# Kernel optimization log

Measured on AMD Instinct MI355X. Metric: run time of the kernel, lower is better.

The kernel has to match this reference:

```python
import jax, jax.numpy as jnp
import numpy as np

IN_F = 4096
OUT_F = 4096
BATCH = 4096


def _dequantize(q, mn, mx):
    # Faithful to dequantize_to_float32: per-tensor affine using the *observed*
    # integer min/max of the stored tensor.
    q_min = q.min()
    q_max = q.max()
    scale = (mx - mn) / (q_max - q_min).astype(jnp.float32)
    return (q - q_min).astype(jnp.float32) * scale + mn


def setup_inputs() -> dict:
    key = jax.random.key(0)
    k1, k2, k3 = jax.random.split(key, 3)
    x = jax.random.normal(k1, (BATCH, IN_F), dtype=jnp.float32)
    # int8-valued weights/bias stored as int32 (same math; dequant uses tensor min/max)
    weight_q = jax.random.randint(k2, (OUT_F, IN_F), -128, 128, dtype=jnp.int32)
    bias_q = jax.random.randint(k3, (OUT_F,), -128, 128, dtype=jnp.int32)
    # per-tensor float range recorded at quantization time (original scales by 255 first,
    # so these ranges are on the scaled tensor; any floats work for correctness testing)
    weight_min = jnp.float32(-4.2)
    weight_max = jnp.float32(4.5)
    bias_min = jnp.float32(-1.3)
    bias_max = jnp.float32(1.1)
    return {
        "x": x,
        "weight_q": weight_q,
        "bias_q": bias_q,
        "weight_min": weight_min,
        "weight_max": weight_max,
        "bias_min": bias_min,
        "bias_max": bias_max,
    }


def reference(x, weight_q, bias_q, weight_min, weight_max, bias_min, bias_max):
    w = _dequantize(weight_q, weight_min, weight_max)   # [OUT_F, IN_F] fp32
    b = _dequantize(bias_q, bias_min, bias_max)         # [OUT_F] fp32
    # F.linear: x @ W^T + b
    return jnp.einsum("bi,oi->bo", x, w) + b
```

## Files before the change

### kernel.cpp

```cpp
#include <hip/hip_runtime.h>
#include <climits>

#define IN_F 4096
#define OUT_F 4096
#define BATCH 4096
#define NPART 1024

typedef __bf16 bf16x8 __attribute__((ext_vector_type(8)));
typedef float f32x4 __attribute__((ext_vector_type(4)));
typedef unsigned short u16x8 __attribute__((ext_vector_type(8)));

__device__ __forceinline__ unsigned short f2bf_rne(float f) {
  unsigned int u = __float_as_uint(f);
  u += 0x7fffu + ((u >> 16) & 1u);
  return (unsigned short)(u >> 16);
}

__global__ __launch_bounds__(256) void k_convW(const int* __restrict__ q,
                                               unsigned short* __restrict__ qb,
                                               int* __restrict__ pmin,
                                               int* __restrict__ pmax) {
  const int n8 = (OUT_F * IN_F) / 8;
  const int stride = NPART * 256;
  int vmin = INT_MAX, vmax = INT_MIN;
  const int4* q4 = (const int4*)q;
  u16x8* qb8 = (u16x8*)qb;
  for (int i = blockIdx.x * 256 + threadIdx.x; i < n8; i += stride) {
    int4 a = q4[2 * i];
    int4 b = q4[2 * i + 1];
    vmin = min(vmin, min(min(min(a.x, a.y), min(a.z, a.w)),
                         min(min(b.x, b.y), min(b.z, b.w))));
    vmax = max(vmax, max(max(max(a.x, a.y), max(a.z, a.w)),
                         max(max(b.x, b.y), max(b.z, b.w))));
    u16x8 h;
    h[0] = f2bf_rne((float)a.x); h[1] = f2bf_rne((float)a.y);
    h[2] = f2bf_rne((float)a.z); h[3] = f2bf_rne((float)a.w);
    h[4] = f2bf_rne((float)b.x); h[5] = f2bf_rne((float)b.y);
    h[6] = f2bf_rne((float)b.z); h[7] = f2bf_rne((float)b.w);
    qb8[i] = h;
  }
  for (int off = 32; off > 0; off >>= 1) {
    vmin = min(vmin, __shfl_down(vmin, off));
    vmax = max(vmax, __shfl_down(vmax, off));
  }
  __shared__ int rmin[4], rmax[4];
  const int wave = threadIdx.x >> 6;
  if ((threadIdx.x & 63) == 0) { rmin[wave] = vmin; rmax[wave] = vmax; }
  __syncthreads();
  if (threadIdx.x == 0) {
    pmin[blockIdx.x] = min(min(rmin[0], rmin[1]), min(rmin[2], rmin[3]));
    pmax[blockIdx.x] = max(max(rmax[0], rmax[1]), max(rmax[2], rmax[3]));
  }
}

__global__ __launch_bounds__(256) void k_convX(const float* __restrict__ x,
                                               unsigned short* __restrict__ xb,
                                               float* __restrict__ rowsum) {
  const int wave = threadIdx.x >> 6;
  const int lane = threadIdx.x & 63;
  const int row = blockIdx.x * 4 + wave;
  const float4* xr = (const float4*)(x + (size_t)row * IN_F);
  u16x8* xbr = (u16x8*)(xb + (size_t)row * IN_F);
  float s = 0.f;
#pragma unroll
  for (int it = 0; it < IN_F / 8 / 64; ++it) {
    const int i = it * 64 + lane;
    float4 v0 = xr[2 * i];
    float4 v1 = xr[2 * i + 1];
    s += ((v0.x + v0.y) + (v0.z + v0.w)) + ((v1.x + v1.y) + (v1.z + v1.w));
    u16x8 h;
    h[0] = f2bf_rne(v0.x); h[1] = f2bf_rne(v0.y);
    h[2] = f2bf_rne(v0.z); h[3] = f2bf_rne(v0.w);
    h[4] = f2bf_rne(v1.x); h[5] = f2bf_rne(v1.y);
    h[6] = f2bf_rne(v1.z); h[7] = f2bf_rne(v1.w);
    xbr[i] = h;
  }
  for (int off = 32; off > 0; off >>= 1) s += __shfl_down(s, off);
  if (lane == 0) rowsum[row] = s;
}

__global__ __launch_bounds__(256) void k_wmm(const int* __restrict__ q,
                                             int* __restrict__ pmin,
                                             int* __restrict__ pmax) {
  const int n4 = (OUT_F * IN_F) / 4;
  const int stride = gridDim.x * blockDim.x;
  int vmin = INT_MAX, vmax = INT_MIN;
  const int4* q4 = (const int4*)q;
  for (int i = blockIdx.x * blockDim.x + threadIdx.x; i < n4; i += stride) {
    int4 v = q4[i];
    vmin = min(vmin, min(min(v.x, v.y), min(v.z, v.w)));
    vmax = max(vmax, max(max(v.x, v.y), max(v.z, v.w)));
  }
  for (int off = 32; off > 0; off >>= 1) {
    vmin = min(vmin, __shfl_down(vmin, off));
    vmax = max(vmax, __shfl_down(vmax, off));
  }
  __shared__ int rmin[4], rmax[4];
  const int wave = threadIdx.x >> 6;
  if ((threadIdx.x & 63) == 0) { rmin[wave] = vmin; rmax[wave] = vmax; }
  __syncthreads();
  if (threadIdx.x == 0) {
    pmin[blockIdx.x] = min(min(rmin[0], rmin[1]), min(rmin[2], rmin[3]));
    pmax[blockIdx.x] = max(max(rmax[0], rmax[1]), max(rmax[2], rmax[3]));
  }
}

__global__ __launch_bounds__(256) void k_scal(const int* __restrict__ pmin,
                                              const int* __restrict__ pmax, int npart,
                                              const int* __restrict__ bq,
                                              const float* __restrict__ wmn,
                                              const float* __restrict__ wmx,
                                              const float* __restrict__ bmn,
                                              const float* __restrict__ bmx,
                                              float* __restrict__ scal) {
  int vmin = INT_MAX, vmax = INT_MIN;
  for (int i = threadIdx.x; i < npart; i += 256) {
    vmin = min(vmin, pmin[i]);
    vmax = max(vmax, pmax[i]);
  }
  int bmin = INT_MAX, bmaxv = INT_MIN;
  for (int i = threadIdx.x; i < OUT_F; i += 256) {
    int v = bq[i];
    bmin = min(bmin, v);
    bmaxv = max(bmaxv, v);
  }
  for (int off = 32; off > 0; off >>= 1) {
    vmin = min(vmin, __shfl_down(vmin, off));
    vmax = max(vmax, __shfl_down(vmax, off));
    bmin = min(bmin, __shfl_down(bmin, off));
    bmaxv = max(bmaxv, __shfl_down(bmaxv, off));
  }
  __shared__ int r[4][4];
  const int wave = threadIdx.x >> 6;
  if ((threadIdx.x & 63) == 0) {
    r[wave][0] = vmin; r[wave][1] = vmax; r[wave][2] = bmin; r[wave][3] = bmaxv;
  }
  __syncthreads();
  if (threadIdx.x == 0) {
    int qmin = min(min(r[0][0], r[1][0]), min(r[2][0], r[3][0]));
    int qmax = max(max(r[0][1], r[1][1]), max(r[2][1], r[3][1]));
    int qbmin = min(min(r[0][2], r[1][2]), min(r[2][2], r[3][2]));
    int qbmax = max(max(r[0][3], r[1][3]), max(r[2][3], r[3][3]));
    float ws = (*wmx - *wmn) / (float)(qmax - qmin);
    scal[0] = ws;
    scal[1] = *wmn - ws * (float)qmin;
    float bs = (*bmx - *bmn) / (float)(qbmax - qbmin);
    scal[2] = bs;
    scal[3] = *bmn - bs * (float)qbmin;
  }
}

__device__ __forceinline__ void load_lds16(const unsigned short* g, unsigned short* l) {
  __builtin_amdgcn_global_load_lds(
      (const __attribute__((address_space(1))) unsigned int*)g,
      (__attribute__((address_space(3))) unsigned int*)l, 16, 0, 0);
}

#define VMW(n) asm volatile("s_waitcnt vmcnt(" #n ")" ::: "memory")
#define CFENCE asm volatile("" ::: "memory")

#define GITER(C, CA, CB, NA, NB, PF, LDN, CHK)                                      \
  {                                                                                 \
    bf16x8 a2_[4];                                                                  \
    _Pragma("unroll") for (int i = 0; i < 4; ++i)                                   \
        a2_[i] = *(const bf16x8*)&As[(C)][(wm + 64 + i * 16 + r16) * 32 + pc];      \
    if (PF) {                                                                       \
      load_lds16(srcA0 + kb + ((C) + 3) * 32, &As[((C) + 3) & 3][dst0]);            \
      load_lds16(srcA1 + kb + ((C) + 3) * 32, &As[((C) + 3) & 3][dst1]);            \
    }                                                                               \
    __builtin_amdgcn_s_setprio(1);                                                  \
    _Pragma("unroll") for (int mi = 0; mi < 4; ++mi)                                \
        _Pragma("unroll") for (int ni = 0; ni < 4; ++ni)                            \
            acc[mi][ni] = __builtin_amdgcn_mfma_f32_16x16x32_bf16(                  \
                CA[mi], CB[ni], acc[mi][ni], 0, 0, 0);                              \
    __builtin_amdgcn_s_setprio(0);                                                  \
    if (LDN) {                                                                      \
      _Pragma("unroll") for (int i = 0; i < 4; ++i) {                               \
        NA[i] = *(const bf16x8*)&As[((C) + 1) & 3][(wm + i * 16 + r16) * 32 + pc];  \
        NB[i] = *(const bf16x8*)&Bs[((C) + 1) & 3][(wn + i * 16 + r16) * 32 + pc];  \
      }                                                                             \
    }                                                                               \
    if (PF) {                                                                       \
      load_lds16(srcB0 + kb + ((C) + 3) * 32, &Bs[((C) + 3) & 3][dst0]);            \
      load_lds16(srcB1 + kb + ((C) + 3) * 32, &Bs[((C) + 3) & 3][dst1]);            \
    }                                                                               \
    __builtin_amdgcn_s_setprio(1);                                                  \
    _Pragma("unroll") for (int mi = 0; mi < 4; ++mi)                                \
        _Pragma("unroll") for (int ni = 0; ni < 4; ++ni)                            \
            acc[4 + mi][ni] = __builtin_amdgcn_mfma_f32_16x16x32_bf16(              \
                a2_[mi], CB[ni], acc[4 + mi][ni], 0, 0, 0);                         \
    __builtin_amdgcn_s_setprio(0);                                                  \
    CHK;                                                                            \
    __builtin_amdgcn_s_barrier();                                                   \
    CFENCE;                                                                         \
  }

__global__ __launch_bounds__(512, 2) void k_gemm(
    const unsigned short* __restrict__ A,
    const unsigned short* __restrict__ B,
    const int* __restrict__ bq,
    const float* __restrict__ rowsum,
    const int* __restrict__ pmin,
    const int* __restrict__ pmax,
    const float* __restrict__ wmn, const float* __restrict__ wmx,
    const float* __restrict__ bmn, const float* __restrict__ bmx,
    float* __restrict__ C) {
  __shared__ __align__(16) unsigned short As[4][8192];
  __shared__ __align__(16) unsigned short Bs[4][8192];
  __shared__ int rr[8][4];
  __shared__ float s_scal[4];

  const int tid = threadIdx.x;
  const int w = tid >> 6;
  const int lane = tid & 63;
  const int bm = blockIdx.x * 256;
  const int bn = blockIdx.y * 256;

  {
    int vmin = INT_MAX, vmax = INT_MIN;
    for (int i = tid; i < NPART; i += 512) {
      vmin = min(vmin, pmin[i]);
      vmax = max(vmax, pmax[i]);
    }
    int bmn_ = INT_MAX, bmx_ = INT_MIN;
    for (int i = tid; i < OUT_F; i += 512) {
      int v = bq[i];
      bmn_ = min(bmn_, v);
      bmx_ = max(bmx_, v);
    }
    for (int off = 32; off > 0; off >>= 1) {
      vmin = min(vmin, __shfl_down(vmin, off));
      vmax = max(vmax, __shfl_down(vmax, off));
      bmn_ = min(bmn_, __shfl_down(bmn_, off));
      bmx_ = max(bmx_, __shfl_down(bmx_, off));
    }
    if ((tid & 63) == 0) { rr[w][0] = vmin; rr[w][1] = vmax; rr[w][2] = bmn_; rr[w][3] = bmx_; }
    __syncthreads();
    if (tid == 0) {
      int qmin = rr[0][0], qmax = rr[0][1], qbmin = rr[0][2], qbmax = rr[0][3];
      for (int i = 1; i < 8; ++i) {
        qmin = min(qmin, rr[i][0]); qmax = max(qmax, rr[i][1]);
        qbmin = min(qbmin, rr[i][2]); qbmax = max(qbmax, rr[i][3]);
      }
      float ws = (*wmx - *wmn) / (float)(qmax - qmin);
      s_scal[0] = ws;
      s_scal[1] = *wmn - ws * (float)qmin;
      float bs = (*bmx - *bmn) / (float)(qbmax - qbmin);
      s_scal[2] = bs;
      s_scal[3] = *bmn - bs * (float)qbmin;
    }
  }

  const int wm = (w & 1) * 128;
  const int wn = (w >> 1) * 64;
  const int r16 = lane & 15;
  const int q = lane >> 4;
  const int pc = (q ^ ((r16 >> 1) & 3)) * 8;

  const int cA0 = w * 128 + lane;
  const int rowS0 = cA0 >> 2;
  const int colS0 = ((cA0 & 3) ^ ((rowS0 >> 1) & 3)) * 8;
  const int cA1 = cA0 + 64;
  const int rowS1 = cA1 >> 2;
  const int colS1 = ((cA1 & 3) ^ ((rowS1 >> 1) & 3)) * 8;
  const unsigned short* srcA0 = A + (size_t)(bm + rowS0) * IN_F + colS0;
  const unsigned short* srcA1 = A + (size_t)(bm + rowS1) * IN_F + colS1;
  const unsigned short* srcB0 = B + (size_t)(bn + rowS0) * IN_F + colS0;
  const unsigned short* srcB1 = B + (size_t)(bn + rowS1) * IN_F + colS1;
  const int dst0 = w * 1024;
  const int dst1 = w * 1024 + 512;

  f32x4 acc[8][4] = {};
  bf16x8 fa0[4], fb0[4], fa1[4], fb1[4];

#pragma unroll
  for (int t = 0; t < 3; ++t) {
    load_lds16(srcA0 + t * 32, &As[t][dst0]);
    load_lds16(srcA1 + t * 32, &As[t][dst1]);
    load_lds16(srcB0 + t * 32, &Bs[t][dst0]);
    load_lds16(srcB1 + t * 32, &Bs[t][dst1]);
  }
  VMW(4);
  __builtin_amdgcn_s_barrier();
  CFENCE;
#pragma unroll
  for (int i = 0; i < 4; ++i) {
    fa0[i] = *(const bf16x8*)&As[0][(wm + i * 16 + r16) * 32 + pc];
    fb0[i] = *(const bf16x8*)&Bs[0][(wn + i * 16 + r16) * 32 + pc];
  }

  for (int u = 0; u < 31; ++u) {
    const int kb = u * 128;
    GITER(0, fa0, fb0, fa1, fb1, 1, 1, VMW(4));
    GITER(1, fa1, fb1, fa0, fb0, 1, 1, VMW(4));
    GITER(2, fa0, fb0, fa1, fb1, 1, 1, VMW(4));
    GITER(3, fa1, fb1, fa0, fb0, 1, 1, VMW(4));
  }
  {
    const int kb = 31 * 128;
    GITER(0, fa0, fb0, fa1, fb1, 1, 1, VMW(4));
    GITER(1, fa1, fb1, fa0, fb0, 0, 1, VMW(0));
    GITER(2, fa0, fb0, fa1, fb1, 0, 1, ((void)0));
    GITER(3, fa1, fb1, fa0, fb0, 0, 0, ((void)0));
  }

  const float wsc = s_scal[0], wbe = s_scal[1], bsc = s_scal[2], bbe = s_scal[3];
#pragma unroll
  for (int ni = 0; ni < 4; ++ni) {
    const int gn = bn + wn + ni * 16 + r16;
    const float bdq = bsc * (float)bq[gn] + bbe;
#pragma unroll
    for (int mi = 0; mi < 8; ++mi) {
      const int gm0 = bm + wm + mi * 16 + q * 4;
#pragma unroll
      for (int r = 0; r < 4; ++r) {
        const int gm = gm0 + r;
        C[(size_t)gm * OUT_F + gn] = wsc * acc[mi][ni][r] + wbe * rowsum[gm] + bdq;
      }
    }
  }
}

__global__ void k_naive(const float* __restrict__ x, const int* __restrict__ wq,
                        const int* __restrict__ bq, const float* __restrict__ scal,
                        float* __restrict__ out) {
  const int o = blockIdx.x * blockDim.x + threadIdx.x;
  const int b = blockIdx.y;
  const float* xr = x + (size_t)b * IN_F;
  const int* wr = wq + (size_t)o * IN_F;
  float s = 0.f, sx = 0.f;
  for (int k = 0; k < IN_F; ++k) {
    float xv = xr[k];
    s += xv * (float)wr[k];
    sx += xv;
  }
  out[(size_t)b * OUT_F + o] =
      scal[0] * s + scal[1] * sx + scal[2] * (float)bq[o] + scal[3];
}

extern "C" void kernel_launch(void* const* d_in, const int* in_sizes, int n_in,
                              void* d_out, int out_size, void* d_ws, size_t ws_size,
                              hipStream_t stream) {
  const float* x = (const float*)d_in[0];
  const int* wq = (const int*)d_in[1];
  const int* bq = (const int*)d_in[2];
  const float* wmn = (const float*)d_in[3];
  const float* wmx = (const float*)d_in[4];
  const float* bmn = (const float*)d_in[5];
  const float* bmx = (const float*)d_in[6];
  float* out = (float*)d_out;

  char* ws = (char*)d_ws;
  float* scal = (float*)ws;
  int* pmin = (int*)(ws + 64);
  int* pmax = (int*)(ws + 64 + NPART * 4);
  float* rowsum = (float*)(ws + 64 + 2 * NPART * 4);
  unsigned short* xb = (unsigned short*)(ws + 32768);
  unsigned short* qb = xb + (size_t)BATCH * IN_F;
  const size_t needed = 32768 + (size_t)BATCH * IN_F * 2 + (size_t)OUT_F * IN_F * 2;

  if (ws_size >= needed) {
    k_convW<<<NPART, 256, 0, stream>>>(wq, qb, pmin, pmax);
    k_convX<<<BATCH / 4, 256, 0, stream>>>(x, xb, rowsum);
    dim3 grid(BATCH / 256, OUT_F / 256);
    k_gemm<<<grid, 512, 0, stream>>>(xb, qb, bq, rowsum, pmin, pmax,
                                     wmn, wmx, bmn, bmx, out);
  } else {
    k_wmm<<<NPART, 256, 0, stream>>>(wq, pmin, pmax);
    k_scal<<<1, 256, 0, stream>>>(pmin, pmax, NPART, bq, wmn, wmx, bmn, bmx, scal);
    k_naive<<<dim3(OUT_F / 256, BATCH), 256, 0, stream>>>(x, wq, bq, scal, out);
  }
}
```

Measured before the change: 316.7 us.

## Fuse weight/activation conversion and GEMM into one persistent kernel with grid barrier

Replaces the three-kernel sequence (weight convert + min/max, activation convert + rowsum, GEMM) with a single 256-block kernel. Each block first converts 16 rows of x and W to bf16, atomically updates the global weight min/max, then waits at a spin-wait grid barrier on an atomic counter before running the GEMM tile. This is meant to remove launch gaps and the tail effects between stages, but it relies on all 256 blocks being co-resident and adds memsets and a spin barrier that has a guard timeout. The bias min/max is now recomputed per block in the epilogue.

```diff
diff --git a/kernel.cpp b/kernel.cpp
--- a/kernel.cpp
+++ b/kernel.cpp
@@ -16,138 +16,19 @@
   return (unsigned short)(u >> 16);
 }
 
-__global__ __launch_bounds__(256) void k_convW(const int* __restrict__ q,
-                                               unsigned short* __restrict__ qb,
-                                               int* __restrict__ pmin,
-                                               int* __restrict__ pmax) {
-  const int n8 = (OUT_F * IN_F) / 8;
-  const int stride = NPART * 256;
-  int vmin = INT_MAX, vmax = INT_MIN;
-  const int4* q4 = (const int4*)q;
-  u16x8* qb8 = (u16x8*)qb;
-  for (int i = blockIdx.x * 256 + threadIdx.x; i < n8; i += stride) {
-    int4 a = q4[2 * i];
-    int4 b = q4[2 * i + 1];
-    vmin = min(vmin, min(min(min(a.x, a.y), min(a.z, a.w)),
-                         min(min(b.x, b.y), min(b.z, b.w))));
-    vmax = max(vmax, max(max(max(a.x, a.y), max(a.z, a.w)),
-                         max(max(b.x, b.y), max(b.z, b.w))));
-    u16x8 h;
-    h[0] = f2bf_rne((float)a.x); h[1] = f2bf_rne((float)a.y);
-    h[2] = f2bf_rne((float)a.z); h[3] = f2bf_rne((float)a.w);
-    h[4] = f2bf_rne((float)b.x); h[5] = f2bf_rne((float)b.y);
-    h[6] = f2bf_rne((float)b.z); h[7] = f2bf_rne((float)b.w);
-    qb8[i] = h;
-  }
-  for (int off = 32; off > 0; off >>= 1) {
-    vmin = min(vmin, __shfl_down(vmin, off));
-    vmax = max(vmax, __shfl_down(vmax, off));
-  }
-  __shared__ int rmin[4], rmax[4];
-  const int wave = threadIdx.x >> 6;
-  if ((threadIdx.x & 63) == 0) { rmin[wave] = vmin; rmax[wave] = vmax; }
-  __syncthreads();
-  if (threadIdx.x == 0) {
-    pmin[blockIdx.x] = min(min(rmin[0], rmin[1]), min(rmin[2], rmin[3]));
-    pmax[blockIdx.x] = max(max(rmax[0], rmax[1]), max(rmax[2], rmax[3]));
-  }
-}
-
-__global__ __launch_bounds__(256) void k_convX(const float* __restrict__ x,
-                                               unsigned short* __restrict__ xb,
-                                               float* __restrict__ rowsum) {
-  const int wave = threadIdx.x >> 6;
-  const int lane = threadIdx.x & 63;
-  const int row = blockIdx.x * 4 + wave;
-  const float4* xr = (const float4*)(x + (size_t)row * IN_F);
-  u16x8* xbr = (u16x8*)(xb + (size_t)row * IN_F);
-  float s = 0.f;
-#pragma unroll
-  for (int it = 0; it < IN_F / 8 / 64; ++it) {
-    const int i = it * 64 + lane;
-    float4 v0 = xr[2 * i];
-    float4 v1 = xr[2 * i + 1];
-    s += ((v0.x + v0.y) + (v0.z + v0.w)) + ((v1.x + v1.y) + (v1.z + v1.w));
-    u16x8 h;
-    h[0] = f2bf_rne(v0.x); h[1] = f2bf_rne(v0.y);
-    h[2] = f2bf_rne(v0.z); h[3] = f2bf_rne(v0.w);
-    h[4] = f2bf_rne(v1.x); h[5] = f2bf_rne(v1.y);
-    h[6] = f2bf_rne(v1.z); h[7] = f2bf_rne(v1.w);
-    xbr[i] = h;
-  }
-  for (int off = 32; off > 0; off >>= 1) s += __shfl_down(s, off);
-  if (lane == 0) rowsum[row] = s;
-}
-
-__global__ __launch_bounds__(256) void k_wmm(const int* __restrict__ q,
-                                             int* __restrict__ pmin,
-                                             int* __restrict__ pmax) {
-  const int n4 = (OUT_F * IN_F) / 4;
-  const int stride = gridDim.x * blockDim.x;
-  int vmin = INT_MAX, vmax = INT_MIN;
-  const int4* q4 = (const int4*)q;
-  for (int i = blockIdx.x * blockDim.x + threadIdx.x; i < n4; i += stride) {
-    int4 v = q4[i];
-    vmin = min(vmin, min(min(v.x, v.y), min(v.z, v.w)));
-    vmax = max(vmax, max(max(v.x, v.y), max(v.z, v.w)));
-  }
-  for (int off = 32; off > 0; off >>= 1) {
-    vmin = min(vmin, __shfl_down(vmin, off));
-    vmax = max(vmax, __shfl_down(vmax, off));
-  }
-  __shared__ int rmin[4], rmax[4];
-  const int wave = threadIdx.x >> 6;
-  if ((threadIdx.x & 63) == 0) { rmin[wave] = vmin; rmax[wave] = vmax; }
-  __syncthreads();
-  if (threadIdx.x == 0) {
-    pmin[blockIdx.x] = min(min(rmin[0], rmin[1]), min(rmin[2], rmin[3]));
-    pmax[blockIdx.x] = max(max(rmax[0], rmax[1]), max(rmax[2], rmax[3]));
-  }
-}
-
-__global__ __launch_bounds__(256) void k_scal(const int* __restrict__ pmin,
-                                              const int* __restrict__ pmax, int npart,
-                                              const int* __restrict__ bq,
-                                              const float* __restrict__ wmn,
-                                              const float* __restrict__ wmx,
-                                              const float* __restrict__ bmn,
-                                              const float* __restrict__ bmx,
-                                              float* __restrict__ scal) {
-  int vmin = INT_MAX, vmax = INT_MIN;
-  for (int i = threadIdx.x; i < npart; i += 256) {
-    vmin = min(vmin, pmin[i]);
-    vmax = max(vmax, pmax[i]);
-  }
-  int bmin = INT_MAX, bmaxv = INT_MIN;
-  for (int i = threadIdx.x; i < OUT_F; i += 256) {
-    int v = bq[i];
-    bmin = min(bmin, v);
-    bmaxv = max(bmaxv, v);
-  }
-  for (int off = 32; off > 0; off >>= 1) {
-    vmin = min(vmin, __shfl_down(vmin, off));
-    vmax = max(vmax, __shfl_down(vmax, off));
-    bmin = min(bmin, __shfl_down(bmin, off));
-    bmaxv = max(bmaxv, __shfl_down(bmaxv, off));
-  }
-  __shared__ int r[4][4];
-  const int wave = threadIdx.x >> 6;
-  if ((threadIdx.x & 63) == 0) {
-    r[wave][0] = vmin; r[wave][1] = vmax; r[wave][2] = bmin; r[wave][3] = bmaxv;
-  }
-  __syncthreads();
-  if (threadIdx.x == 0) {
-    int qmin = min(min(r[0][0], r[1][0]), min(r[2][0], r[3][0]));
-    int qmax = max(max(r[0][1], r[1][1]), max(r[2][1], r[3][1]));
-    int qbmin = min(min(r[0][2], r[1][2]), min(r[2][2], r[3][2]));
-    int qbmax = max(max(r[0][3], r[1][3]), max(r[2][3], r[3][3]));
-    float ws = (*wmx - *wmn) / (float)(qmax - qmin);
-    scal[0] = ws;
-    scal[1] = *wmn - ws * (float)qmin;
-    float bs = (*bmx - *bmn) / (float)(qbmax - qbmin);
-    scal[2] = bs;
-    scal[3] = *bmn - bs * (float)qbmin;
-  }
+__device__ __forceinline__ u16x8 cvt8f(float4 a, float4 b) {
+  u16x8 h;
+  h[0] = f2bf_rne(a.x); h[1] = f2bf_rne(a.y); h[2] = f2bf_rne(a.z); h[3] = f2bf_rne(a.w);
+  h[4] = f2bf_rne(b.x); h[5] = f2bf_rne(b.y); h[6] = f2bf_rne(b.z); h[7] = f2bf_rne(b.w);
+  return h;
+}
+__device__ __forceinline__ u16x8 cvt8i(int4 a, int4 b) {
+  u16x8 h;
+  h[0] = f2bf_rne((float)a.x); h[1] = f2bf_rne((float)a.y);
+  h[2] = f2bf_rne((float)a.z); h[3] = f2bf_rne((float)a.w);
+  h[4] = f2bf_rne((float)b.x); h[5] = f2bf_rne((float)b.y);
+  h[6] = f2bf_rne((float)b.z); h[7] = f2bf_rne((float)b.w);
+  return h;
 }
 
 __device__ __forceinline__ void load_lds16(const unsigned short* g, unsigned short* l) {
@@ -195,61 +76,84 @@
     CFENCE;                                                                         \
   }
 
-__global__ __launch_bounds__(512, 2) void k_gemm(
-    const unsigned short* __restrict__ A,
-    const unsigned short* __restrict__ B,
+__global__ __launch_bounds__(512, 2) void k_fused(
+    const float* __restrict__ X,
+    const int* __restrict__ WQ,
     const int* __restrict__ bq,
-    const float* __restrict__ rowsum,
-    const int* __restrict__ pmin,
-    const int* __restrict__ pmax,
     const float* __restrict__ wmn, const float* __restrict__ wmx,
     const float* __restrict__ bmn, const float* __restrict__ bmx,
+    unsigned short* __restrict__ xb,
+    unsigned short* __restrict__ qb,
+    float* __restrict__ rowsum,
+    int* __restrict__ qminw, int* __restrict__ qmaxw,
+    unsigned int* __restrict__ ctr,
     float* __restrict__ C) {
   __shared__ __align__(16) unsigned short As[4][8192];
   __shared__ __align__(16) unsigned short Bs[4][8192];
-  __shared__ int rr[8][4];
-  __shared__ float s_scal[4];
 
   const int tid = threadIdx.x;
   const int w = tid >> 6;
   const int lane = tid & 63;
-  const int bm = blockIdx.x * 256;
-  const int bn = blockIdx.y * 256;
+  const int bid = blockIdx.x;
 
   {
     int vmin = INT_MAX, vmax = INT_MIN;
-    for (int i = tid; i < NPART; i += 512) {
-      vmin = min(vmin, pmin[i]);
-      vmax = max(vmax, pmax[i]);
-    }
-    int bmn_ = INT_MAX, bmx_ = INT_MIN;
-    for (int i = tid; i < OUT_F; i += 512) {
-      int v = bq[i];
-      bmn_ = min(bmn_, v);
-      bmx_ = max(bmx_, v);
+#pragma unroll
+    for (int rr = 0; rr < 2; ++rr) {
+      const int row = bid * 16 + w * 2 + rr;
+      const float4* xr = (const float4*)(X + (size_t)row * IN_F);
+      u16x8* xbr = (u16x8*)(xb + (size_t)row * IN_F);
+      float s = 0.f;
+#pragma unroll
+      for (int it = 0; it < IN_F / 8 / 64; ++it) {
+        const int i = it * 64 + lane;
+        float4 v0 = xr[2 * i];
+        float4 v1 = xr[2 * i + 1];
+        s += ((v0.x + v0.y) + (v0.z + v0.w)) + ((v1.x + v1.y) + (v1.z + v1.w));
+        xbr[i] = cvt8f(v0, v1);
+      }
+      for (int off = 32; off > 0; off >>= 1) s += __shfl_down(s, off);
+      if (lane == 0) rowsum[row] = s;
+      const int4* qr = (const int4*)(WQ + (size_t)row * IN_F);
+      u16x8* qbr = (u16x8*)(qb + (size_t)row * IN_F);
+#pragma unroll
+      for (int it = 0; it < IN_F / 8 / 64; ++it) {
+        const int i = it * 64 + lane;
+        int4 a = qr[2 * i];
+        int4 b = qr[2 * i + 1];
+        vmin = min(vmin, min(min(min(a.x, a.y), min(a.z, a.w)),
+                             min(min(b.x, b.y), min(b.z, b.w))));
+        vmax = max(vmax, max(max(max(a.x, a.y), max(a.z, a.w)),
+                             max(max(b.x, b.y), max(b.z, b.w))));
+        qbr[i] = cvt8i(a, b);
+      }
     }
     for (int off = 32; off > 0; off >>= 1) {
       vmin = min(vmin, __shfl_down(vmin, off));
       vmax = max(vmax, __shfl_down(vmax, off));
-      bmn_ = min(bmn_, __shfl_down(bmn_, off));
-      bmx_ = max(bmx_, __shfl_down(bmx_, off));
-    }
-    if ((tid & 63) == 0) { rr[w][0] = vmin; rr[w][1] = vmax; rr[w][2] = bmn_; rr[w][3] = bmx_; }
-    __syncthreads();
-    if (tid == 0) {
-      int qmin = rr[0][0], qmax = rr[0][1], qbmin = rr[0][2], qbmax = rr[0][3];
-      for (int i = 1; i < 8; ++i) {
-        qmin = min(qmin, rr[i][0]); qmax = max(qmax, rr[i][1]);
-        qbmin = min(qbmin, rr[i][2]); qbmax = max(qbmax, rr[i][3]);
-      }
-      float ws = (*wmx - *wmn) / (float)(qmax - qmin);
-      s_scal[0] = ws;
-      s_scal[1] = *wmn - ws * (float)qmin;
-      float bs = (*bmx - *bmn) / (float)(qbmax - qbmin);
-      s_scal[2] = bs;
-      s_scal[3] = *bmn - bs * (float)qbmin;
-    }
-  }
+    }
+    if (lane == 0) {
+      atomicMin(qminw, vmin);
+      atomicMax(qmaxw, vmax);
+    }
+  }
+
+  __threadfence();
+  __syncthreads();
+  if (tid == 0) {
+    __hip_atomic_fetch_add(ctr, 1u, __ATOMIC_RELEASE, __HIP_MEMORY_SCOPE_AGENT);
+    int guard = 0;
+    while (__hip_atomic_load(ctr, __ATOMIC_ACQUIRE, __HIP_MEMORY_SCOPE_AGENT) < 256u &&
+           guard < 2000000) {
+      __builtin_amdgcn_s_sleep(2);
+      ++guard;
+    }
+  }
+  __syncthreads();
+  (void)__hip_atomic_load(ctr, __ATOMIC_ACQUIRE, __HIP_MEMORY_SCOPE_AGENT);
+
+  const int bm = (bid & 15) * 256;
+  const int bn = (bid >> 4) * 256;
 
   const int wm = (w & 1) * 128;
   const int wn = (w >> 1) * 64;
@@ -263,10 +167,10 @@
   const int cA1 = cA0 + 64;
   const int rowS1 = cA1 >> 2;
   const int colS1 = ((cA1 & 3) ^ ((rowS1 >> 1) & 3)) * 8;
-  const unsigned short* srcA0 = A + (size_t)(bm + rowS0) * IN_F + colS0;
-  const unsigned short* srcA1 = A + (size_t)(bm + rowS1) * IN_F + colS1;
-  const unsigned short* srcB0 = B + (size_t)(bn + rowS0) * IN_F + colS0;
-  const unsigned short* srcB1 = B + (size_t)(bn + rowS1) * IN_F + colS1;
+  const unsigned short* srcA0 = xb + (size_t)(bm + rowS0) * IN_F + colS0;
+  const unsigned short* srcA1 = xb + (size_t)(bm + rowS1) * IN_F + colS1;
+  const unsigned short* srcB0 = qb + (size_t)(bn + rowS0) * IN_F + colS0;
+  const unsigned short* srcB1 = qb + (size_t)(bn + rowS1) * IN_F + colS1;
   const int dst0 = w * 1024;
   const int dst1 = w * 1024 + 512;
 
@@ -304,7 +208,32 @@
     GITER(3, fa1, fb1, fa0, fb0, 0, 0, ((void)0));
   }
 
-  const float wsc = s_scal[0], wbe = s_scal[1], bsc = s_scal[2], bbe = s_scal[3];
+  const int qmin = *qminw;
+  const int qmax = *qmaxw;
+  const float wsc = (*wmx - *wmn) / (float)(qmax - qmin);
+  const float wbe = *wmn - wsc * (float)qmin;
+  int bmin_ = INT_MAX, bmax_ = INT_MIN;
+  for (int i = tid; i < OUT_F; i += 512) {
+    int v = bq[i];
+    bmin_ = min(bmin_, v);
+    bmax_ = max(bmax_, v);
+  }
+  for (int off = 32; off > 0; off >>= 1) {
+    bmin_ = min(bmin_, __shfl_down(bmin_, off));
+    bmax_ = max(bmax_, __shfl_down(bmax_, off));
+  }
+  __shared__ int rbr[8][2];
+  if (lane == 0) { rbr[w][0] = bmin_; rbr[w][1] = bmax_; }
+  __syncthreads();
+  int qbmin = rbr[0][0], qbmax = rbr[0][1];
+#pragma unroll
+  for (int i = 1; i < 8; ++i) {
+    qbmin = min(qbmin, rbr[i][0]);
+    qbmax = max(qbmax, rbr[i][1]);
+  }
+  const float bsc = (*bmx - *bmn) / (float)(qbmax - qbmin);
+  const float bbe = *bmn - bsc * (float)qbmin;
+
 #pragma unroll
   for (int ni = 0; ni < 4; ++ni) {
     const int gn = bn + wn + ni * 16 + r16;
@@ -318,6 +247,77 @@
         C[(size_t)gm * OUT_F + gn] = wsc * acc[mi][ni][r] + wbe * rowsum[gm] + bdq;
       }
     }
+  }
+}
+
+__global__ __launch_bounds__(256) void k_wmm(const int* __restrict__ q,
+                                             int* __restrict__ pmin,
+                                             int* __restrict__ pmax) {
+  const int n4 = (OUT_F * IN_F) / 4;
+  const int stride = gridDim.x * blockDim.x;
+  int vmin = INT_MAX, vmax = INT_MIN;
+  const int4* q4 = (const int4*)q;
+  for (int i = blockIdx.x * blockDim.x + threadIdx.x; i < n4; i += stride) {
+    int4 v = q4[i];
+    vmin = min(vmin, min(min(v.x, v.y), min(v.z, v.w)));
+    vmax = max(vmax, max(max(v.x, v.y), max(v.z, v.w)));
+  }
+  for (int off = 32; off > 0; off >>= 1) {
+    vmin = min(vmin, __shfl_down(vmin, off));
+    vmax = max(vmax, __shfl_down(vmax, off));
+  }
+  __shared__ int rmin[4], rmax[4];
+  const int wave = threadIdx.x >> 6;
+  if ((threadIdx.x & 63) == 0) { rmin[wave] = vmin; rmax[wave] = vmax; }
+  __syncthreads();
+  if (threadIdx.x == 0) {
+    pmin[blockIdx.x] = min(min(rmin[0], rmin[1]), min(rmin[2], rmin[3]));
+    pmax[blockIdx.x] = max(max(rmax[0], rmax[1]), max(rmax[2], rmax[3]));
+  }
+}
+
+__global__ __launch_bounds__(256) void k_scal(const int* __restrict__ pmin,
+                                              const int* __restrict__ pmax, int npart,
+                                              const int* __restrict__ bq,
+                                              const float* __restrict__ wmn,
+                                              const float* __restrict__ wmx,
+                                              const float* __restrict__ bmn,
+                                              const float* __restrict__ bmx,
+                                              float* __restrict__ scal) {
+  int vmin = INT_MAX, vmax = INT_MIN;
+  for (int i = threadIdx.x; i < npart; i += 256) {
+    vmin = min(vmin, pmin[i]);
+    vmax = max(vmax, pmax[i]);
+  }
+  int bmin = INT_MAX, bmaxv = INT_MIN;
+  for (int i = threadIdx.x; i < OUT_F; i += 256) {
+    int v = bq[i];
+    bmin = min(bmin, v);
+    bmaxv = max(bmaxv, v);
+  }
+  for (int off = 32; off > 0; off >>= 1) {
+    vmin = min(vmin, __shfl_down(vmin, off));
+    vmax = max(vmax, __shfl_down(vmax, off));
+    bmin = min(bmin, __shfl_down(bmin, off));
+    bmaxv = max(bmaxv, __shfl_down(bmaxv, off));
+  }
+  __shared__ int r[4][4];
+  const int wave = threadIdx.x >> 6;
+  if ((threadIdx.x & 63) == 0) {
+    r[wave][0] = vmin; r[wave][1] = vmax; r[wave][2] = bmin; r[wave][3] = bmaxv;
+  }
+  __syncthreads();
+  if (threadIdx.x == 0) {
+    int qmin = min(min(r[0][0], r[1][0]), min(r[2][0], r[3][0]));
+    int qmax = max(max(r[0][1], r[1][1]), max(r[2][1], r[3][1]));
+    int qbmin = min(min(r[0][2], r[1][2]), min(r[2][2], r[3][2]));
+    int qbmax = max(max(r[0][3], r[1][3]), max(r[2][3], r[3][3]));
+    float ws = (*wmx - *wmn) / (float)(qmax - qmin);
+    scal[0] = ws;
+    scal[1] = *wmn - ws * (float)qmin;
+    float bs = (*bmx - *bmn) / (float)(qbmax - qbmin);
+    scal[2] = bs;
+    scal[3] = *bmn - bs * (float)qbmin;
   }
 }
 
@@ -351,20 +351,23 @@
   float* out = (float*)d_out;
 
   char* ws = (char*)d_ws;
-  float* scal = (float*)ws;
-  int* pmin = (int*)(ws + 64);
-  int* pmax = (int*)(ws + 64 + NPART * 4);
-  float* rowsum = (float*)(ws + 64 + 2 * NPART * 4);
+  unsigned int* ctr = (unsigned int*)ws;
+  int* qminw = (int*)(ws + 16);
+  int* qmaxw = (int*)(ws + 20);
+  float* scal = (float*)(ws + 32);
+  float* rowsum = (float*)(ws + 64);
+  int* pmin = (int*)(ws + 16448);
+  int* pmax = (int*)(ws + 16448 + NPART * 4);
   unsigned short* xb = (unsigned short*)(ws + 32768);
   unsigned short* qb = xb + (size_t)BATCH * IN_F;
   const size_t needed = 32768 + (size_t)BATCH * IN_F * 2 + (size_t)OUT_F * IN_F * 2;
 
   if (ws_size >= needed) {
-    k_convW<<<NPART, 256, 0, stream>>>(wq, qb, pmin, pmax);
-    k_convX<<<BATCH / 4, 256, 0, stream>>>(x, xb, rowsum);
-    dim3 grid(BATCH / 256, OUT_F / 256);
-    k_gemm<<<grid, 512, 0, stream>>>(xb, qb, bq, rowsum, pmin, pmax,
-                                     wmn, wmx, bmn, bmx, out);
+    hipMemsetAsync(ctr, 0, 4, stream);
+    hipMemsetAsync(qminw, 0x7f, 4, stream);
+    hipMemsetAsync(qmaxw, 0x80, 4, stream);
+    k_fused<<<256, 512, 0, stream>>>(x, wq, bq, wmn, wmx, bmn, bmx,
+                                     xb, qb, rowsum, qminw, qmaxw, ctr, out);
   } else {
     k_wmm<<<NPART, 256, 0, stream>>>(wq, pmin, pmax);
     k_scal<<<1, 256, 0, stream>>>(pmin, pmax, NPART, bq, wmn, wmx, bmn, bmx, scal);
```

After: 453.8 us. +43.3%, slower.
